# Kernel tuning notes

Measured on AMD Instinct MI355X. Metric: run time of the kernel, lower is better.

## Reference

```python
import jax, jax.numpy as jnp
import numpy as np
from jax import lax

NUM_HEADS = 8
NUM_LAYERS = 3


def _conv3d(x, w, b):
    # x: [B,C,D,H,W], w: [O,I,3,3,3] (torch Conv3d layout), padding=1, stride=1
    y = lax.conv_general_dilated(x, w, window_strides=(1, 1, 1),
                                 padding=[(1, 1)] * 3,
                                 dimension_numbers=('NCDHW', 'OIDHW', 'NCDHW'))
    return y + b[None, :, None, None, None]


def _attn(x, wq, bq, wk, bk, wv, bv, gamma):
    # Faithful translation of MultiHeadAttentionModule.forward
    B, C, D, H, W = x.shape
    N = D * H * W
    hd = C // NUM_HEADS
    scale = jnp.asarray(hd ** 0.5, x.dtype)
    xf = x.reshape(B, C, N).transpose(0, 2, 1)  # [B,N,C]

    def proj(wm, bm):
        # torch Linear: y = x @ W.T + b ; split C -> (heads, head_dim)
        return (xf @ wm.T + bm).reshape(B, N, NUM_HEADS, hd).transpose(0, 2, 1, 3)

    q = proj(wq, bq)  # [B,h,N,d]
    k = proj(wk, bk)
    v = proj(wv, bv)
    energy = jnp.einsum('bhnd,bhmd->bhnm', q, k) / scale  # [B,h,N,N]
    attn = jax.nn.softmax(energy, axis=-1)
    o = jnp.einsum('bhnm,bhmd->bhnd', attn, v)  # [B,h,N,d]
    # permute(0,1,3,2).view(in_shape): channel order is (head, head_dim)
    o = o.transpose(0, 1, 3, 2).reshape(B, C, D, H, W)
    return gamma * o + x


def setup_inputs() -> dict:
    key = jax.random.key(0)
    ks = jax.random.split(key, 16)
    B, Cin, D, H, W = 1, 64, 16, 16, 16
    Co = 128
    L = NUM_LAYERS
    s = 0.02
    return {
        'x': jax.random.normal(ks[0], (B, Cin, D, H, W), jnp.float32),
        'lateral_w': jax.random.normal(ks[1], (Co, Cin, 3, 3, 3), jnp.float32) * s,
        'lateral_b': jax.random.normal(ks[2], (Co,), jnp.float32) * s,
        'pos': jax.random.normal(ks[3], (1, Co, D, H, W), jnp.float32) * s,
        'qw': jax.random.normal(ks[4], (L, Co, Co), jnp.float32) * s,
        'qb': jax.random.normal(ks[5], (L, Co), jnp.float32) * s,
        'kw': jax.random.normal(ks[6], (L, Co, Co), jnp.float32) * s,
        'kb': jax.random.normal(ks[7], (L, Co), jnp.float32) * s,
        'vw': jax.random.normal(ks[8], (L, Co, Co), jnp.float32) * s,
        'vb': jax.random.normal(ks[9], (L, Co), jnp.float32) * s,
        'gamma': jnp.full((L,), 0.5, jnp.float32),
        'out_w': jax.random.normal(ks[10], (Co, Co, 3, 3, 3), jnp.float32) * s,  # ConvTranspose3d weight [in,out,k,k,k]
        'out_b': jax.random.normal(ks[11], (Co,), jnp.float32) * s,
    }


def reference(x, lateral_w, lateral_b, pos, qw, qb, kw, kb, vw, vb, gamma, out_w, out_b):
    # t_dim == 1 branch of FPN3DWithMultiHeadAttention.forward
    lat = _conv3d(x, lateral_w, lateral_b) + pos
    for i in range(NUM_LAYERS):
        lat = _attn(lat, qw[i], qb[i], kw[i], kb[i], vw[i], vb[i], gamma[i])
    # ConvTranspose3d(k=3, stride=1, pad=1) == Conv3d with spatially flipped,
    # channel-transposed kernel and padding k-1-p = 1
    w_eq = jnp.flip(out_w, axis=(2, 3, 4)).transpose(1, 0, 2, 3, 4)
    return _conv3d(lat, w_eq, out_b)
```

## Files before the change

### kernel.cpp

```cpp
#include <hip/hip_runtime.h>
#include <hip/hip_bf16.h>

#define NVOX 4096
#define CDIM 128

typedef __attribute__((ext_vector_type(8)))  short bf16x8;
typedef __attribute__((ext_vector_type(4)))  float f32x4;
typedef __attribute__((ext_vector_type(16))) float f32x16;

static __device__ __forceinline__ short f2bf(float f) {
    __hip_bfloat16 h = __float2bfloat16(f);
    union { __hip_bfloat16 h; short s; } u; u.h = h; return u.s;
}
static __device__ __forceinline__ float fexp2(float x) {
    return __builtin_amdgcn_exp2f(x);
}
__device__ __forceinline__ int permpos(int ci) {
    return (((ci >> 2) & 3) << 3) + (ci & 3) + ((ci & 16) >> 2) + ((ci >> 5) << 5);
}
__device__ __forceinline__ int invp(int p) {
    const int c = p >> 5, r = p & 31, g = (r >> 3) & 3, j = r & 7;
    return (c << 5) + (j < 4 ? (g << 2) + j : 16 + (g << 2) + (j - 4));
}
__device__ __forceinline__ int pos16(int d) {
    return (d & 3) | ((d & 4) << 1) | ((d & 8) >> 1);
}

__global__ __launch_bounds__(256) void pack_all(
    const float* __restrict__ x,  const float* __restrict__ lw,
    const float* __restrict__ qw, const float* __restrict__ kw, const float* __restrict__ vw,
    const float* __restrict__ ow,
    short* __restrict__ xp, short* __restrict__ wb1, short* __restrict__ wqkv, short* __restrict__ wb2)
{
    const int b = blockIdx.x;
    const int tid = threadIdx.x;
    if (b < 1458) {
        const int e = b * 256 + tid;
        if (e >= 5832 * 64) return;
        const int vp = e >> 6, p = e & 63;
        const int z = vp / 324, rem = vp - z * 324, y = rem / 18, xx = rem % 18;
        short val = 0;
        if (z >= 1 && z <= 16 && y >= 1 && y <= 16 && xx >= 1 && xx <= 16) {
            const int n = ((z - 1) * 16 + (y - 1)) * 16 + (xx - 1);
            val = f2bf(x[invp(p) * NVOX + n]);
        }
        xp[e] = val;
    } else if (b < 1458 + 864) {
        const int e = (b - 1458) * 256 + tid;
        if (e >= 27 * 128 * 64) return;
        const int t = e >> 13, co = (e >> 6) & 127, p = e & 63;
        wb1[e] = f2bf(lw[(co * 64 + invp(p)) * 27 + t]);
    } else if (b < 1458 + 864 + 576) {
        const int e = (b - 2322) * 256 + tid;
        if (e >= 3 * 3 * 128 * 128) return;
        const int l = e / 49152, r = e - l * 49152;
        const int m = r >> 14, co = (r >> 7) & 127, p = r & 127;
        const float* W = (m == 0 ? qw : m == 1 ? kw : vw) + l * 16384;
        wqkv[e] = f2bf(W[co * 128 + invp(p)]);
    } else {
        const int e = (b - 2898) * 256 + tid;
        if (e >= 27 * 128 * 128) return;
        const int t = e >> 14, co = (e >> 7) & 127, p = e & 127;
        wb2[e] = f2bf(ow[(invp(p) * 128 + co) * 27 + (26 - t)]);
    }
}

__global__ __launch_bounds__(256) void pad2_kernel(const short* __restrict__ latbf, short* __restrict__ xp) {
    const int e = blockIdx.x * 256 + threadIdx.x;
    if (e >= 5832 * 16) return;
    const int vp = e >> 4, c8 = e & 15;
    const int z = vp / 324, rem = vp - z * 324, y = rem / 18, xx = rem % 18;
    int4 val = {0, 0, 0, 0};
    if (z >= 1 && z <= 16 && y >= 1 && y <= 16 && xx >= 1 && xx <= 16) {
        const int n = ((z - 1) * 16 + (y - 1)) * 16 + (xx - 1);
        val = *reinterpret_cast<const int4*>(latbf + n * 128 + c8 * 8);
    }
    *reinterpret_cast<int4*>(xp + vp * 128 + c8 * 8) = val;
}

__global__ __launch_bounds__(256) void conv1_mfma(
    const short* __restrict__ xp,
    const short* __restrict__ wb,
    const float* __restrict__ bias, const float* __restrict__ pos,
    float* __restrict__ lat, short* __restrict__ latbf)
{
    __shared__ short bl[324 * 72];
    const int tid = threadIdx.x;
    const int g = blockIdx.x;
    const int cot = g >> 6;
    const int vgrp = g & 63;
    const int r0 = vgrp * 4;
    const int z = r0 >> 4, y0 = r0 & 15;

    for (int i = tid; i < 2592; i += 256) {
        const int col = i >> 3, pc = i & 7;
        const int line = col / 18, xq = col - line * 18;
        const int dz = line / 6, yi = line - dz * 6;
        const int4 v = *reinterpret_cast<const int4*>(
            xp + (((z + dz) * 18 + (y0 + yi)) * 18 + xq) * 64 + pc * 8);
        const int slot = ((((pc >> 2) ^ col) & 1) << 5) + ((pc & 3) << 3);
        *reinterpret_cast<int4*>(&bl[col * 72 + slot]) = v;
    }
    __syncthreads();

    const int wid = tid >> 6, lane = tid & 63;
    const int lg = lane >> 4, lq = lane & 15;
    const int wc = wid >> 1, wv = wid & 1;
    const int co0 = cot * 32 + wc * 16;

    const short* pA = wb + (co0 + lq) * 64 + lg * 8;

    auto ldA = [&](int t, bf16x8* A) {
        const short* p = pA + t * 8192;
        #pragma unroll
        for (int c = 0; c < 2; ++c) A[c] = *reinterpret_cast<const bf16x8*>(p + c * 32);
    };

    f32x4 acc0 = {0.f,0.f,0.f,0.f}, acc1 = {0.f,0.f,0.f,0.f};

    auto comp = [&](int t, const bf16x8* A) {
        const int dz = t / 9, r9 = t - dz * 9, dy = r9 / 3, dx = r9 - dy * 3;
        #pragma unroll
        for (int ry = 0; ry < 2; ++ry) {
            const int col = (dz * 6 + wv * 2 + ry + dy) * 18 + dx + lq;
            const short* bp = &bl[col * 72 + (lg << 3)];
            #pragma unroll
            for (int c = 0; c < 2; ++c) {
                const bf16x8 b = *reinterpret_cast<const bf16x8*>(bp + (((c ^ col) & 1) << 5));
                if (ry == 0) acc0 = __builtin_amdgcn_mfma_f32_16x16x32_bf16(A[c], b, acc0, 0, 0, 0);
                else         acc1 = __builtin_amdgcn_mfma_f32_16x16x32_bf16(A[c], b, acc1, 0, 0, 0);
            }
        }
    };

    bf16x8 A0[2], A1[2];
    int t = 0;
    ldA(0, A0);
    while (true) {
        if (t + 1 < 27) ldA(t + 1, A1);
        comp(t, A0);
        if (++t >= 27) break;
        if (t + 1 < 27) ldA(t + 1, A0);
        comp(t, A1);
        if (++t >= 27) break;
    }

    #pragma unroll
    for (int ry = 0; ry < 2; ++ry) {
        const f32x4 a = ry ? acc1 : acc0;
        const int n = (r0 + wv * 2 + ry) * 16 + lq;
        short4 s4;
        #pragma unroll
        for (int i = 0; i < 4; ++i) {
            const int co = co0 + 4 * lg + i;
            const float v = a[i] + bias[co] + pos[co * NVOX + n];
            lat[co * NVOX + n] = v;
            ((short*)&s4)[i] = f2bf(v);
        }
        *reinterpret_cast<short4*>(latbf + n * 128 + permpos(co0 + 4 * lg)) = s4;
    }
}

__global__ __launch_bounds__(256) void proj_mfma(
    const short* __restrict__ latbf,
    const short* __restrict__ wl,
    const float* __restrict__ bq, const float* __restrict__ bk, const float* __restrict__ bv,
    short* __restrict__ qP, short* __restrict__ kP, short* __restrict__ vP)
{
    const int m = blockIdx.z;
    const int wid = threadIdx.x >> 6, lane = threadIdx.x & 63;
    const int lg = lane >> 4, lq = lane & 15;
    const int co0 = blockIdx.y * 16;
    const int row0 = (blockIdx.x * 4 + wid) * 2;

    const short* A = wl + m * 16384 + (co0 + lq) * 128 + lg * 8;
    bf16x8 Af[4];
    #pragma unroll
    for (int c = 0; c < 4; ++c) Af[c] = *reinterpret_cast<const bf16x8*>(A + c * 32);

    const short* Bp0 = latbf + (row0 * 16 + lq) * 128 + lg * 8;
    const short* Bp1 = Bp0 + 16 * 128;
    bf16x8 Bf0[4], Bf1[4];
    #pragma unroll
    for (int c = 0; c < 4; ++c) Bf0[c] = *reinterpret_cast<const bf16x8*>(Bp0 + c * 32);
    #pragma unroll
    for (int c = 0; c < 4; ++c) Bf1[c] = *reinterpret_cast<const bf16x8*>(Bp1 + c * 32);

    f32x4 a0a = {0.f,0.f,0.f,0.f}, a0b = a0a, a1a = a0a, a1b = a0a;
    a0a = __builtin_amdgcn_mfma_f32_16x16x32_bf16(Af[0], Bf0[0], a0a, 0, 0, 0);
    a1a = __builtin_amdgcn_mfma_f32_16x16x32_bf16(Af[0], Bf1[0], a1a, 0, 0, 0);
    a0b = __builtin_amdgcn_mfma_f32_16x16x32_bf16(Af[1], Bf0[1], a0b, 0, 0, 0);
    a1b = __builtin_amdgcn_mfma_f32_16x16x32_bf16(Af[1], Bf1[1], a1b, 0, 0, 0);
    a0a = __builtin_amdgcn_mfma_f32_16x16x32_bf16(Af[2], Bf0[2], a0a, 0, 0, 0);
    a1a = __builtin_amdgcn_mfma_f32_16x16x32_bf16(Af[2], Bf1[2], a1a, 0, 0, 0);
    a0b = __builtin_amdgcn_mfma_f32_16x16x32_bf16(Af[3], Bf0[3], a0b, 0, 0, 0);
    a1b = __builtin_amdgcn_mfma_f32_16x16x32_bf16(Af[3], Bf1[3], a1b, 0, 0, 0);

    const int h = blockIdx.y;
    #pragma unroll
    for (int rr = 0; rr < 2; ++rr) {
        const f32x4 acc = rr ? (a1a + a1b) : (a0a + a0b);
        const int row = row0 + rr;
        const int n = row * 16 + lq;
        if (m == 2) {
            const int col = row * 16 + pos16(lq);
            #pragma unroll
            for (int r = 0; r < 4; ++r) {
                const int d = lg * 4 + r;
                vP[(h * 17 + d) * NVOX + col] = f2bf(acc[r] + bv[co0 + d]);
            }
            if (lg == 0) vP[(h * 17 + 16) * NVOX + col] = (short)0x3F80;
        } else {
            const float* bias = (m == 0) ? bq : bk;
            const float S = (m == 0) ? 0.25f * 1.4426950408889634f : 1.f;
            const int pg = ((lg & 1) << 3) | ((lg & 2) << 1);
            short4 s4;
            #pragma unroll
            for (int r = 0; r < 4; ++r) {
                const int co = co0 + lg * 4 + r;
                ((short*)&s4)[r] = f2bf((acc[r] + bias[co]) * S);
            }
            short* dst = (m == 0) ? qP : kP;
            *reinterpret_cast<short4*>(dst + ((h << 12) + n) * 16 + pg) = s4;
        }
    }
}

__global__ __launch_bounds__(256) void attn_mfma(
    const short* __restrict__ qP, const short* __restrict__ kP, const short* __restrict__ vP,
    const float* __restrict__ latin, float* __restrict__ latout, short* __restrict__ latbf,
    const float* __restrict__ gamma, int layer)
{
    __shared__ float smO[4][64][17];
    const int tid = threadIdx.x;
    const int wid = tid >> 6, lane = tid & 63;
    const int l5 = lane >> 5, lm = lane & 31;
    const int h = blockIdx.y;
    const int qbase = blockIdx.x * 64;

    const bf16x8 qf0 = *reinterpret_cast<const bf16x8*>(
        qP + (((h << 12) + qbase + lm) << 4) + l5 * 8);
    const bf16x8 qf1 = *reinterpret_cast<const bf16x8*>(
        qP + (((h << 12) + qbase + 32 + lm) << 4) + l5 * 8);

    const short* kbase = kP + (((size_t)h) << 16);
    const int vrow = (lm & 16) ? 16 : lm;
    const short* vbase = vP + ((size_t)h * 17 + vrow) * NVOX + l5 * 8;

    f32x16 acc0 = {0.f,0.f,0.f,0.f,0.f,0.f,0.f,0.f,0.f,0.f,0.f,0.f,0.f,0.f,0.f,0.f};
    f32x16 acc1 = acc0;
    const f32x16 zero = acc0;

    bf16x8 kfA, v0A, v1A, kfB, v0B, v1B;
    auto LD = [&](int kc, bf16x8& kf, bf16x8& v0, bf16x8& v1) {
        kf = *reinterpret_cast<const bf16x8*>(kbase + ((kc + lm) << 4) + l5 * 8);
        v0 = *reinterpret_cast<const bf16x8*>(vbase + kc);
        v1 = *reinterpret_cast<const bf16x8*>(vbase + kc + 16);
    };
    auto COMP = [&](const bf16x8& kf, const bf16x8& v0, const bf16x8& v1) {
        const f32x16 S0 = __builtin_amdgcn_mfma_f32_32x32x16_bf16(kf, qf0, zero, 0, 0, 0);
        const f32x16 S1 = __builtin_amdgcn_mfma_f32_32x32x16_bf16(kf, qf1, zero, 0, 0, 0);
        short p0[16], p1[16];
        #pragma unroll
        for (int r = 0; r < 16; ++r) p0[r] = f2bf(fexp2(S0[r]));
        #pragma unroll
        for (int r = 0; r < 16; ++r) p1[r] = f2bf(fexp2(S1[r]));
        const bf16x8 pa00 = {p0[0],p0[1],p0[2],p0[3],p0[4],p0[5],p0[6],p0[7]};
        const bf16x8 pa01 = {p0[8],p0[9],p0[10],p0[11],p0[12],p0[13],p0[14],p0[15]};
        const bf16x8 pa10 = {p1[0],p1[1],p1[2],p1[3],p1[4],p1[5],p1[6],p1[7]};
        const bf16x8 pa11 = {p1[8],p1[9],p1[10],p1[11],p1[12],p1[13],p1[14],p1[15]};
        acc0 = __builtin_amdgcn_mfma_f32_32x32x16_bf16(pa00, v0, acc0, 0, 0, 0);
        acc0 = __builtin_amdgcn_mfma_f32_32x32x16_bf16(pa01, v1, acc0, 0, 0, 0);
        acc1 = __builtin_amdgcn_mfma_f32_32x32x16_bf16(pa10, v0, acc1, 0, 0, 0);
        acc1 = __builtin_amdgcn_mfma_f32_32x32x16_bf16(pa11, v1, acc1, 0, 0, 0);
    };

    int kc = wid * 1024;
    int it = 0;
    LD(kc, kfA, v0A, v1A);
    while (true) {
        if (it + 1 < 32) LD(kc + 32, kfB, v0B, v1B);
        COMP(kfA, v0A, v1A);
        kc += 32;
        if (++it >= 32) break;
        if (it + 1 < 32) LD(kc + 32, kfA, v0A, v1A);
        COMP(kfB, v0B, v1B);
        kc += 32;
        if (++it >= 32) break;
    }

    if (lm <= 16) {
        #pragma unroll
        for (int r = 0; r < 16; ++r) {
            const int qrow = (r & 3) + 8 * (r >> 2) + 4 * l5;
            smO[wid][qrow][lm]      = acc0[r];
            smO[wid][32 + qrow][lm] = acc1[r];
        }
    }
    __syncthreads();

    const int q = tid >> 2;
    const int d0 = (tid & 3) * 4;
    const float ls = smO[0][q][16] + smO[1][q][16] + smO[2][q][16] + smO[3][q][16];
    const float ginv = gamma[layer] / ls;
    const int n = qbase + q;
    short4 s4;
    #pragma unroll
    for (int dd = 0; dd < 4; ++dd) {
        const int d = d0 + dd;
        const float Ov = smO[0][q][d] + smO[1][q][d] + smO[2][q][d] + smO[3][q][d];
        const int c = (h << 4) + d;
        const float val = Ov * ginv + latin[c * NVOX + n];
        latout[c * NVOX + n] = val;
        ((short*)&s4)[dd] = f2bf(val);
    }
    *reinterpret_cast<short4*>(latbf + n * 128 + permpos((h << 4) + d0)) = s4;
}

__global__ __launch_bounds__(256) void conv2_mfma(
    const short* __restrict__ xp,
    const short* __restrict__ wb,
    const float* __restrict__ bias,
    float* __restrict__ out)
{
    __shared__ short bl[324 * 136];
    const int tid = threadIdx.x;
    const int g = blockIdx.x;
    const int cot = g >> 6;
    const int vgrp = g & 63;
    const int r0 = vgrp * 4;
    const int z = r0 >> 4, y0 = r0 & 15;

    for (int i = tid; i < 5184; i += 256) {
        const int col = i >> 4, pc = i & 15;
        const int line = col / 18, xq = col - line * 18;
        const int dz = line / 6, yi = line - dz * 6;
        const int4 v = *reinterpret_cast<const int4*>(
            xp + (((z + dz) * 18 + (y0 + yi)) * 18 + xq) * 128 + pc * 8);
        const int slot = ((((pc >> 2) ^ col) & 3) << 5) + ((pc & 3) << 3);
        *reinterpret_cast<int4*>(&bl[col * 136 + slot]) = v;
    }
    __syncthreads();

    const int wid = tid >> 6, lane = tid & 63;
    const int lg = lane >> 4, lq = lane & 15;
    const int wc = wid >> 1, wv = wid & 1;
    const int co0 = cot * 32 + wc * 16;

    const short* pA = wb + (co0 + lq) * 128 + lg * 8;

    auto ldA = [&](int t, bf16x8* A) {
        const short* p = pA + t * 16384;
        #pragma unroll
        for (int c = 0; c < 4; ++c) A[c] = *reinterpret_cast<const bf16x8*>(p + c * 32);
    };

    f32x4 acc0 = {0.f,0.f,0.f,0.f}, acc1 = {0.f,0.f,0.f,0.f};

    auto comp = [&](int t, const bf16x8* A) {
        const int dz = t / 9, r9 = t - dz * 9, dy = r9 / 3, dx = r9 - dy * 3;
        #pragma unroll
        for (int ry = 0; ry < 2; ++ry) {
            const int col = (dz * 6 + wv * 2 + ry + dy) * 18 + dx + lq;
            const short* bp = &bl[col * 136 + (lg << 3)];
            #pragma unroll
            for (int c = 0; c < 4; ++c) {
                const bf16x8 b = *reinterpret_cast<const bf16x8*>(bp + (((c ^ col) & 3) << 5));
                if (ry == 0) acc0 = __builtin_amdgcn_mfma_f32_16x16x32_bf16(A[c], b, acc0, 0, 0, 0);
                else         acc1 = __builtin_amdgcn_mfma_f32_16x16x32_bf16(A[c], b, acc1, 0, 0, 0);
            }
        }
    };

    bf16x8 A0[4], A1[4];
    int t = 0;
    ldA(0, A0);
    while (true) {
        if (t + 1 < 27) ldA(t + 1, A1);
        comp(t, A0);
        if (++t >= 27) break;
        if (t + 1 < 27) ldA(t + 1, A0);
        comp(t, A1);
        if (++t >= 27) break;
    }

    #pragma unroll
    for (int ry = 0; ry < 2; ++ry) {
        const f32x4 a = ry ? acc1 : acc0;
        const int n = (r0 + wv * 2 + ry) * 16 + lq;
        #pragma unroll
        for (int i = 0; i < 4; ++i) {
            const int co = co0 + 4 * lg + i;
            out[co * NVOX + n] = a[i] + bias[co];
        }
    }
}

extern "C" void kernel_launch(void* const* d_in, const int* in_sizes, int n_in,
                              void* d_out, int out_size, void* d_ws, size_t ws_size,
                              hipStream_t stream) {
    const float* x     = (const float*)d_in[0];
    const float* lw    = (const float*)d_in[1];
    const float* lb    = (const float*)d_in[2];
    const float* pos   = (const float*)d_in[3];
    const float* qw    = (const float*)d_in[4];
    const float* qb    = (const float*)d_in[5];
    const float* kw    = (const float*)d_in[6];
    const float* kb    = (const float*)d_in[7];
    const float* vw    = (const float*)d_in[8];
    const float* vb    = (const float*)d_in[9];
    const float* gamma = (const float*)d_in[10];
    const float* ow    = (const float*)d_in[11];
    const float* ob    = (const float*)d_in[12];

    float* latA  = (float*)d_ws;
    float* latB  = latA + 524288;
    short* latbf = (short*)(latB + 524288);
    short* qP    = latbf + 524288;
    short* kP    = qP + 524288;
    short* vP    = kP + 524288;
    short* xpad  = vP + 557056;
    short* wbf1  = xpad + 746496;
    short* wqkv  = wbf1 + 221184;
    short* wbf2  = wqkv + 442368;

    pack_all<<<4626, 256, 0, stream>>>(x, lw, qw, kw, vw, ow, xpad, wbf1, wqkv, wbf2);

    conv1_mfma<<<256, 256, 0, stream>>>(xpad, wbf1, lb, pos, latA, latbf);

    float* cur = latA;
    float* nxt = latB;
    for (int i = 0; i < 3; ++i) {
        proj_mfma<<<dim3(32, 8, 3), 256, 0, stream>>>(
            latbf, wqkv + i * 49152, qb + i * 128, kb + i * 128, vb + i * 128, qP, kP, vP);
        attn_mfma<<<dim3(64, 8), 256, 0, stream>>>(qP, kP, vP, cur, nxt, latbf, gamma, i);
        float* t = cur; cur = nxt; nxt = t;
    }

    pad2_kernel<<<365, 256, 0, stream>>>(latbf, xpad);
    conv2_mfma<<<256, 256, 0, stream>>>(xpad, wbf2, ob, (float*)d_out);
}
```

Baseline: 148.6 us.

## Fuse conv2 padding into last attention layer and widen attention blocks

Result: faster. 126.8 us (-14.6%).

```diff
diff --git a/kernel.cpp b/kernel.cpp
--- a/kernel.cpp
+++ b/kernel.cpp
@@ -30,7 +30,8 @@
     const float* __restrict__ x,  const float* __restrict__ lw,
     const float* __restrict__ qw, const float* __restrict__ kw, const float* __restrict__ vw,
     const float* __restrict__ ow,
-    short* __restrict__ xp, short* __restrict__ wb1, short* __restrict__ wqkv, short* __restrict__ wb2)
+    short* __restrict__ xp, short* __restrict__ wb1, short* __restrict__ wqkv, short* __restrict__ wb2,
+    short* __restrict__ xp2)
 {
     const int b = blockIdx.x;
     const int tid = threadIdx.x;
@@ -57,25 +58,17 @@
         const int m = r >> 14, co = (r >> 7) & 127, p = r & 127;
         const float* W = (m == 0 ? qw : m == 1 ? kw : vw) + l * 16384;
         wqkv[e] = f2bf(W[co * 128 + invp(p)]);
-    } else {
+    } else if (b < 1458 + 864 + 576 + 1728) {
         const int e = (b - 2898) * 256 + tid;
         if (e >= 27 * 128 * 128) return;
         const int t = e >> 14, co = (e >> 7) & 127, p = e & 127;
         wb2[e] = f2bf(ow[(invp(p) * 128 + co) * 27 + (26 - t)]);
-    }
-}
-
-__global__ __launch_bounds__(256) void pad2_kernel(const short* __restrict__ latbf, short* __restrict__ xp) {
-    const int e = blockIdx.x * 256 + threadIdx.x;
-    if (e >= 5832 * 16) return;
-    const int vp = e >> 4, c8 = e & 15;
-    const int z = vp / 324, rem = vp - z * 324, y = rem / 18, xx = rem % 18;
-    int4 val = {0, 0, 0, 0};
-    if (z >= 1 && z <= 16 && y >= 1 && y <= 16 && xx >= 1 && xx <= 16) {
-        const int n = ((z - 1) * 16 + (y - 1)) * 16 + (xx - 1);
-        val = *reinterpret_cast<const int4*>(latbf + n * 128 + c8 * 8);
-    }
-    *reinterpret_cast<int4*>(xp + vp * 128 + c8 * 8) = val;
+    } else {
+        const int e = (b - 4626) * 256 + tid;
+        if (e >= 5832 * 16) return;
+        const int4 z4 = {0, 0, 0, 0};
+        *reinterpret_cast<int4*>(xp2 + e * 8) = z4;
+    }
 }
 
 __global__ __launch_bounds__(256) void conv1_mfma(
@@ -226,17 +219,18 @@
     }
 }
 
-__global__ __launch_bounds__(256) void attn_mfma(
+__global__ __launch_bounds__(512) void attn_mfma(
     const short* __restrict__ qP, const short* __restrict__ kP, const short* __restrict__ vP,
-    const float* __restrict__ latin, float* __restrict__ latout, short* __restrict__ latbf,
-    const float* __restrict__ gamma, int layer)
+    const float* __restrict__ latin, float* __restrict__ latout, short* __restrict__ outbf,
+    const float* __restrict__ gamma, int layer, int last)
 {
-    __shared__ float smO[4][64][17];
+    __shared__ float smO[8][64][17];
     const int tid = threadIdx.x;
     const int wid = tid >> 6, lane = tid & 63;
     const int l5 = lane >> 5, lm = lane & 31;
+    const int qg = wid >> 2, ksp = wid & 3;
     const int h = blockIdx.y;
-    const int qbase = blockIdx.x * 64;
+    const int qbase = blockIdx.x * 128 + qg * 64;
 
     const bf16x8 qf0 = *reinterpret_cast<const bf16x8*>(
         qP + (((h << 12) + qbase + lm) << 4) + l5 * 8);
@@ -275,7 +269,7 @@
         acc1 = __builtin_amdgcn_mfma_f32_32x32x16_bf16(pa11, v1, acc1, 0, 0, 0);
     };
 
-    int kc = wid * 1024;
+    int kc = ksp * 1024;
     int it = 0;
     LD(kc, kfA, v0A, v1A);
     while (true) {
@@ -301,20 +295,27 @@
 
     const int q = tid >> 2;
     const int d0 = (tid & 3) * 4;
-    const float ls = smO[0][q][16] + smO[1][q][16] + smO[2][q][16] + smO[3][q][16];
+    const int g4 = (q >> 6) * 4, ql = q & 63;
+    const float ls = smO[g4][ql][16] + smO[g4+1][ql][16] + smO[g4+2][ql][16] + smO[g4+3][ql][16];
     const float ginv = gamma[layer] / ls;
-    const int n = qbase + q;
+    const int n = blockIdx.x * 128 + q;
     short4 s4;
     #pragma unroll
     for (int dd = 0; dd < 4; ++dd) {
         const int d = d0 + dd;
-        const float Ov = smO[0][q][d] + smO[1][q][d] + smO[2][q][d] + smO[3][q][d];
+        const float Ov = smO[g4][ql][d] + smO[g4+1][ql][d] + smO[g4+2][ql][d] + smO[g4+3][ql][d];
         const int c = (h << 4) + d;
         const float val = Ov * ginv + latin[c * NVOX + n];
-        latout[c * NVOX + n] = val;
+        if (!last) latout[c * NVOX + n] = val;
         ((short*)&s4)[dd] = f2bf(val);
     }
-    *reinterpret_cast<short4*>(latbf + n * 128 + permpos((h << 4) + d0)) = s4;
+    if (!last) {
+        *reinterpret_cast<short4*>(outbf + n * 128 + permpos((h << 4) + d0)) = s4;
+    } else {
+        const int zq = n >> 8, yq = (n >> 4) & 15, xq = n & 15;
+        const int vp = (zq + 1) * 324 + (yq + 1) * 18 + (xq + 1);
+        *reinterpret_cast<short4*>(outbf + vp * 128 + permpos((h << 4) + d0)) = s4;
+    }
 }
 
 __global__ __launch_bounds__(256) void conv2_mfma(
@@ -420,23 +421,25 @@
     short* kP    = qP + 524288;
     short* vP    = kP + 524288;
     short* xpad  = vP + 557056;
-    short* wbf1  = xpad + 746496;
+    short* xpad2 = xpad + 373248;
+    short* wbf1  = xpad2 + 746496;
     short* wqkv  = wbf1 + 221184;
     short* wbf2  = wqkv + 442368;
 
-    pack_all<<<4626, 256, 0, stream>>>(x, lw, qw, kw, vw, ow, xpad, wbf1, wqkv, wbf2);
+    pack_all<<<4809, 256, 0, stream>>>(x, lw, qw, kw, vw, ow, xpad, wbf1, wqkv, wbf2, xpad2);
 
     conv1_mfma<<<256, 256, 0, stream>>>(xpad, wbf1, lb, pos, latA, latbf);
 
     float* cur = latA;
     float* nxt = latB;
     for (int i = 0; i < 3; ++i) {
+        const int last = (i == 2);
         proj_mfma<<<dim3(32, 8, 3), 256, 0, stream>>>(
             latbf, wqkv + i * 49152, qb + i * 128, kb + i * 128, vb + i * 128, qP, kP, vP);
-        attn_mfma<<<dim3(64, 8), 256, 0, stream>>>(qP, kP, vP, cur, nxt, latbf, gamma, i);
+        attn_mfma<<<dim3(32, 8), 512, 0, stream>>>(
+            qP, kP, vP, cur, nxt, last ? xpad2 : latbf, gamma, i, last);
         float* t = cur; cur = nxt; nxt = t;
     }
 
-    pad2_kernel<<<365, 256, 0, stream>>>(latbf, xpad);
-    conv2_mfma<<<256, 256, 0, stream>>>(xpad, wbf2, ob, (float*)d_out);
-}
+    conv2_mfma<<<256, 256, 0, stream>>>(xpad2, wbf2, ob, (float*)d_out);
+}
```
